# Kernel tuning notes

Hardware: AMD Instinct MI355X
Metric: run time of the kernel (lower is better)

## Reference

```python
import jax, jax.numpy as jnp
import numpy as np
import math

N_HEADS = 16


def setup_inputs() -> dict:
    key = jax.random.key(0)
    ks = jax.random.split(key, 8)
    B, N, H = 4, 1024, 1024
    hidden_states = jax.random.normal(ks[0], (B, N, H), dtype=jnp.float32)
    # per-sample valid length in [N//2, N]; padding_vector is nonzero on valid
    # positions, zero afterwards (first zero index defines the pad boundary)
    lengths = jax.random.randint(ks[1], (B,), N // 2, N + 1)
    padding_vector = (jnp.arange(N)[None, :] < lengths[:, None]).astype(jnp.int32)
    s = 0.02
    Wq = jax.random.normal(ks[2], (H, H), dtype=jnp.float32) * s
    Wk = jax.random.normal(ks[3], (H, H), dtype=jnp.float32) * s
    Wv = jax.random.normal(ks[4], (H, H), dtype=jnp.float32) * s
    bq = jnp.zeros((H,), dtype=jnp.float32)
    bk = jnp.zeros((H,), dtype=jnp.float32)
    bv = jnp.zeros((H,), dtype=jnp.float32)
    return dict(hidden_states=hidden_states, padding_vector=padding_vector,
                Wq=Wq, bq=bq, Wk=Wk, bk=bk, Wv=Wv, bv=bv, max_n_codes=N)


def _heads(x, n_heads):
    B, N, H = x.shape
    return x.reshape(B, N, n_heads, H // n_heads).transpose(0, 2, 1, 3)  # (B,h,N,d)


def reference(hidden_states, padding_vector, Wq, bq, Wk, bk, Wv, bv, max_n_codes):
    B, N, H = hidden_states.shape
    d = H // N_HEADS
    q = _heads(hidden_states @ Wq.T + bq, N_HEADS)  # (B,h,N,d)
    k = _heads(hidden_states @ Wk.T + bk, N_HEADS)
    v = _heads(hidden_states @ Wv.T + bv, N_HEADS)
    scores = jnp.einsum('bhnd,bhmd->bhnm', q, k) / math.sqrt(d)
    # padd = index of first zero in padding_vector, or N if no zero
    is_zero = padding_vector == 0
    padd = jnp.where(is_zero.any(axis=1), jnp.argmax(is_zero, axis=1), N)  # (B,)
    idx = jnp.arange(N)
    valid = idx[None, :] < padd[:, None]                      # (B,N)
    keep = valid[:, None, :, None] & valid[:, None, None, :]  # (B,1,N,N)
    # masked positions get -inf pre-softmax, then are zeroed post-softmax.
    # finfo.min instead of -inf keeps fully-masked rows NaN-free; they are
    # zeroed by the post-softmax mask exactly as in the torch version.
    neg = jnp.finfo(scores.dtype).min
    probs = jax.nn.softmax(jnp.where(keep, scores, neg), axis=-1)
    probs = jnp.where(keep, probs, 0.0)
    attention_values = probs.sum(axis=-2)                     # (B,h,N)
    context = jnp.einsum('bhnm,bhmd->bhnd', probs, v)
    return (attention_values, k, q, context, scores)
```

## Files before the change

kernel.cpp:

```cpp
#include <hip/hip_runtime.h>
#include <math.h>

#define B_ 4
#define N_ 1024
#define H_ 1024
#define NH_ 16
#define D_ 64

#define SZ_ATTN (B_*NH_*N_)
#define SZ_HEADS (B_*NH_*N_*D_)

#define XT_CHUNKS (32*16*1024)
#define WT_CHUNKS (8*16*1024)

typedef __attribute__((ext_vector_type(8))) short short8v;
typedef __attribute__((ext_vector_type(4))) short short4v;
typedef __attribute__((ext_vector_type(4))) float floatx4;

typedef __attribute__((address_space(1))) const unsigned int gau32;
typedef __attribute__((address_space(3))) unsigned int lau32;

__device__ inline void gl16(const unsigned short* g, unsigned short* l) {
    __builtin_amdgcn_global_load_lds((gau32*)g, (lau32*)l, 16, 0, 0);
}

__device__ inline unsigned short f2bf(float x) {
    union { float f; unsigned int u; } v; v.f = x;
    unsigned int r = v.u + 0x7FFFu + ((v.u >> 16) & 1u);
    return (unsigned short)(r >> 16);
}
__device__ inline float bf2f(unsigned short u) {
    union { unsigned int i; float f; } v; v.i = ((unsigned int)u) << 16;
    return v.f;
}

__global__ void padd_kernel(const int* __restrict__ pv, int* __restrict__ padd) {
    __shared__ int mn;
    const int b = blockIdx.x;
    if (threadIdx.x == 0) mn = N_;
    __syncthreads();
    for (int m = threadIdx.x; m < N_; m += blockDim.x)
        if (pv[b*N_ + m] == 0) atomicMin(&mn, m);
    __syncthreads();
    if (threadIdx.x == 0) padd[b] = mn;
}

__global__ __launch_bounds__(256)
void convert_kernel(const float* __restrict__ X,  const float* __restrict__ Wq,
                    const float* __restrict__ Wk, const float* __restrict__ Wv,
                    unsigned short* __restrict__ scratch)
{
    const int g = blockIdx.x*256 + threadIdx.x;
    const float* src;
    if (g < XT_CHUNKS) {
        const int c = g & 1023, t = g >> 10;
        const int it = t >> 4, kt = t & 15;
        const int row = c >> 3, kcs = c & 7, kc = kcs ^ (row & 7);
        src = X + (size_t)(it*128 + row)*H_ + kt*64 + kc*8;
    } else {
        const int gw = g - XT_CHUNKS;
        const int which = gw >> 17;
        const int rem = gw & (WT_CHUNKS-1);
        const int c = rem & 1023, t = rem >> 10;
        const int jt = t >> 4, kt = t & 15;
        const int row = c >> 3, kcs = c & 7, kc = kcs ^ (row & 7);
        const float* W = (which == 0) ? Wq : (which == 1) ? Wk : Wv;
        src = W + (size_t)(jt*128 + row)*H_ + kt*64 + kc*8;
    }
    const float4 a = *(const float4*)src;
    const float4 b = *(const float4*)(src + 4);
    short8v pk;
    pk[0] = (short)f2bf(a.x); pk[1] = (short)f2bf(a.y);
    pk[2] = (short)f2bf(a.z); pk[3] = (short)f2bf(a.w);
    pk[4] = (short)f2bf(b.x); pk[5] = (short)f2bf(b.y);
    pk[6] = (short)f2bf(b.z); pk[7] = (short)f2bf(b.w);
    *(short8v*)(scratch + (size_t)g*8) = pk;
}

__global__ __launch_bounds__(256)
void proj3_mfma_kernel(const unsigned short* __restrict__ Xt,
                       const unsigned short* __restrict__ Wt_all,
                       const float* __restrict__ bq_, const float* __restrict__ bk_,
                       const float* __restrict__ bv_,
                       float* __restrict__ Oq, float* __restrict__ Ok,
                       float* __restrict__ Ov)
{
    const int which = blockIdx.z;
    const unsigned short* __restrict__ Wt = Wt_all + (size_t)which*WT_CHUNKS*8;
    const float* __restrict__ bias = (which == 0) ? bq_ : (which == 1) ? bk_ : bv_;
    float* __restrict__ outH       = (which == 0) ? Oq  : (which == 1) ? Ok  : Ov;

    __shared__ __align__(16) unsigned short Abf[128*64];
    __shared__ __align__(16) unsigned short Bbf[128*64];

    const int tid  = threadIdx.x;
    const int lane = tid & 63;
    const int w    = tid >> 6;
    const int wr   = w >> 1, wc = w & 1;
    const int fr   = lane & 15, hi = lane >> 4;
    const int i0 = blockIdx.y * 128;
    const int j0 = blockIdx.x * 128;

    floatx4 acc[4][4];
    #pragma unroll
    for (int mi = 0; mi < 4; ++mi)
        #pragma unroll
        for (int ni = 0; ni < 4; ++ni)
            acc[mi][ni] = (floatx4){0.f, 0.f, 0.f, 0.f};

    for (int ktile = 0; ktile < 16; ++ktile) {
        __syncthreads();
        const unsigned short* xsrc = Xt + (size_t)(blockIdx.y*16 + ktile)*8192;
        const unsigned short* wsrc = Wt + (size_t)(blockIdx.x*16 + ktile)*8192;
        #pragma unroll
        for (int l = 0; l < 4; ++l) {
            const int ch = l*256 + tid;
            gl16(xsrc + (size_t)ch*8, Abf + (size_t)ch*8);
            gl16(wsrc + (size_t)ch*8, Bbf + (size_t)ch*8);
        }
        __syncthreads();

        #pragma unroll
        for (int ks = 0; ks < 2; ++ks) {
            short8v a[4], b[4];
            #pragma unroll
            for (int mi = 0; mi < 4; ++mi) {
                const int row = wr*64 + mi*16 + fr;
                a[mi] = *(const short8v*)&Abf[row*64 + (((ks*4 + hi) ^ (fr & 7)) << 3)];
            }
            #pragma unroll
            for (int ni = 0; ni < 4; ++ni) {
                const int row = wc*64 + ni*16 + fr;
                b[ni] = *(const short8v*)&Bbf[row*64 + (((ks*4 + hi) ^ (fr & 7)) << 3)];
            }
            #pragma unroll
            for (int mi = 0; mi < 4; ++mi)
                #pragma unroll
                for (int ni = 0; ni < 4; ++ni)
                    acc[mi][ni] = __builtin_amdgcn_mfma_f32_16x16x32_bf16(
                        a[mi], b[ni], acc[mi][ni], 0, 0, 0);
        }
    }

    #pragma unroll
    for (int ni = 0; ni < 4; ++ni) {
        const int j = j0 + wc*64 + ni*16 + fr;
        const int head = j >> 6, d = j & 63;
        const float bvj = bias[j];
        #pragma unroll
        for (int mi = 0; mi < 4; ++mi) {
            #pragma unroll
            for (int reg = 0; reg < 4; ++reg) {
                const int i = i0 + wr*64 + mi*16 + hi*4 + reg;
                const int bb = i >> 10, n = i & 1023;
                outH[((size_t)(bb*NH_ + head)*N_ + n)*D_ + d] = acc[mi][ni][reg] + bvj;
            }
        }
    }
}

__global__ __launch_bounds__(256)
void fused_attn_mfma(const float* __restrict__ Q, const float* __restrict__ K,
                     const float* __restrict__ Vh, const int* __restrict__ padd,
                     float* __restrict__ S, float* __restrict__ ctx,
                     float* __restrict__ attn)
{
    __shared__ __align__(16) unsigned short Abf[128*64];
    __shared__ __align__(16) unsigned short Bbf[64*64];
    __shared__ float smx[128], sinv[128];
    __shared__ float cred[256];

    const int tid  = threadIdx.x;
    const int lane = tid & 63;
    const int w    = tid >> 6;
    const int fr   = lane & 15, hi = lane >> 4;
    const int bh = blockIdx.y;
    const int n0 = blockIdx.x * 128;
    const int b  = bh >> 4;
    const int pd = padd[b];
    const float* Qb = Q  + (size_t)bh*N_*D_;
    const float* Kb = K  + (size_t)bh*N_*D_;
    const float* Vb = Vh + (size_t)bh*N_*D_;
    float* Sb = S + (size_t)bh*N_*N_;

    #pragma unroll
    for (int l = 0; l < 4; ++l) {
        const int e = tid + 256*l;
        const int row = e >> 3, kc = e & 7;
        const float* src = Qb + (size_t)(n0+row)*D_ + kc*8;
        const float4 xa = *(const float4*)(src);
        const float4 xb = *(const float4*)(src + 4);
        short8v pk;
        pk[0] = (short)f2bf(xa.x); pk[1] = (short)f2bf(xa.y);
        pk[2] = (short)f2bf(xa.z); pk[3] = (short)f2bf(xa.w);
        pk[4] = (short)f2bf(xb.x); pk[5] = (short)f2bf(xb.y);
        pk[6] = (short)f2bf(xb.z); pk[7] = (short)f2bf(xb.w);
        *(short8v*)&Abf[row*64 + ((kc ^ (row & 7)) << 3)] = pk;
    }
    __syncthreads();

    short8v qa[2][2];
    #pragma unroll
    for (int mi = 0; mi < 2; ++mi)
        #pragma unroll
        for (int ks = 0; ks < 2; ++ks) {
            const int arow = w*32 + mi*16 + fr;
            qa[mi][ks] = *(const short8v*)&Abf[arow*64 + (((ks*4 + hi) ^ (fr & 7)) << 3)];
        }

    float run_mx[2][4], run_sm[2][4];
    #pragma unroll
    for (int mi = 0; mi < 2; ++mi)
        #pragma unroll
        for (int reg = 0; reg < 4; ++reg) { run_mx[mi][reg] = -INFINITY; run_sm[mi][reg] = 0.f; }

    for (int m0 = 0; m0 < N_; m0 += 64) {
        #pragma unroll
        for (int l = 0; l < 2; ++l) {
            const int e = tid + 256*l;
            const int row = e >> 3, kc = e & 7;
            const float* src = Kb + (size_t)(m0+row)*D_ + kc*8;
            const float4 xa = *(const float4*)(src);
            const float4 xb = *(const float4*)(src + 4);
            short8v pk;
            pk[0] = (short)f2bf(xa.x); pk[1] = (short)f2bf(xa.y);
            pk[2] = (short)f2bf(xa.z); pk[3] = (short)f2bf(xa.w);
            pk[4] = (short)f2bf(xb.x); pk[5] = (short)f2bf(xb.y);
            pk[6] = (short)f2bf(xb.z); pk[7] = (short)f2bf(xb.w);
            *(short8v*)&Bbf[row*64 + ((kc ^ (row & 7)) << 3)] = pk;
        }
        __syncthreads();

        floatx4 sacc[2][4];
        #pragma unroll
        for (int mi = 0; mi < 2; ++mi)
            #pragma unroll
            for (int ni = 0; ni < 4; ++ni)
                sacc[mi][ni] = (floatx4){0.f, 0.f, 0.f, 0.f};

        #pragma unroll
        for (int ks = 0; ks < 2; ++ks) {
            short8v kb[4];
            #pragma unroll
            for (int ni = 0; ni < 4; ++ni) {
                const int brow = ni*16 + fr;
                kb[ni] = *(const short8v*)&Bbf[brow*64 + (((ks*4 + hi) ^ (fr & 7)) << 3)];
            }
            #pragma unroll
            for (int mi = 0; mi < 2; ++mi)
                #pragma unroll
                for (int ni = 0; ni < 4; ++ni)
                    sacc[mi][ni] = __builtin_amdgcn_mfma_f32_16x16x32_bf16(
                        qa[mi][ks], kb[ni], sacc[mi][ni], 0, 0, 0);
        }

        #pragma unroll
        for (int mi = 0; mi < 2; ++mi)
            #pragma unroll
            for (int ni = 0; ni < 4; ++ni) {
                sacc[mi][ni] *= 0.125f;
                const int m = m0 + ni*16 + fr;
                #pragma unroll
                for (int reg = 0; reg < 4; ++reg) {
                    const int n = n0 + w*32 + mi*16 + hi*4 + reg;
                    Sb[(size_t)n*N_ + m] = sacc[mi][ni][reg];
                }
            }

        if (m0 < pd) {
            #pragma unroll
            for (int mi = 0; mi < 2; ++mi)
                #pragma unroll
                for (int reg = 0; reg < 4; ++reg) {
                    float tm = -INFINITY;
                    #pragma unroll
                    for (int ni = 0; ni < 4; ++ni)
                        if (m0 + ni*16 + fr < pd) tm = fmaxf(tm, sacc[mi][ni][reg]);
                    tm = fmaxf(tm, __shfl_xor(tm, 1, 64));
                    tm = fmaxf(tm, __shfl_xor(tm, 2, 64));
                    tm = fmaxf(tm, __shfl_xor(tm, 4, 64));
                    tm = fmaxf(tm, __shfl_xor(tm, 8, 64));
                    const float nm = fmaxf(run_mx[mi][reg], tm);
                    float s = 0.f;
                    #pragma unroll
                    for (int ni = 0; ni < 4; ++ni)
                        if (m0 + ni*16 + fr < pd) s += __expf(sacc[mi][ni][reg] - nm);
                    s += __shfl_xor(s, 1, 64);
                    s += __shfl_xor(s, 2, 64);
                    s += __shfl_xor(s, 4, 64);
                    s += __shfl_xor(s, 8, 64);
                    run_sm[mi][reg] = run_sm[mi][reg]*__expf(run_mx[mi][reg] - nm) + s;
                    run_mx[mi][reg] = nm;
                }
        }
        __syncthreads();
    }

    if (n0 >= pd) {
        #pragma unroll
        for (int l = 0; l < 8; ++l) {
            const int e = tid + 256*l;
            const int row = e >> 4, c4 = e & 15;
            float4 z; z.x = z.y = z.z = z.w = 0.f;
            *(float4*)(ctx + ((size_t)bh*N_ + n0 + row)*D_ + c4*4) = z;
        }
        return;
    }

    if (fr == 0) {
        #pragma unroll
        for (int mi = 0; mi < 2; ++mi)
            #pragma unroll
            for (int reg = 0; reg < 4; ++reg) {
                const int row = w*32 + mi*16 + hi*4 + reg;
                const bool v = (n0 + row) < pd;
                smx[row]  = v ? run_mx[mi][reg] : 0.f;
                sinv[row] = v ? 1.f/run_sm[mi][reg] : 0.f;
            }
    }
    __syncthreads();

    floatx4 acc2[2][4];
    #pragma unroll
    for (int mi = 0; mi < 2; ++mi)
        #pragma unroll
        for (int ni = 0; ni < 4; ++ni)
            acc2[mi][ni] = (floatx4){0.f, 0.f, 0.f, 0.f};

    for (int m0 = 0; m0 < pd; m0 += 64) {
        #pragma unroll
        for (int l = 0; l < 8; ++l) {
            const int e = tid + 256*l;
            const int row = e >> 4, c4 = e & 15;
            const int n = n0 + row;
            const int m = m0 + c4*4;
            const float4 s4 = *(const float4*)(Sb + (size_t)n*N_ + m);
            const bool rv = n < pd;
            const float fmx = smx[row], fiv = sinv[row];
            short4v pk;
            pk[0] = (short)f2bf((rv && m+0 < pd) ? __expf(s4.x - fmx)*fiv : 0.f);
            pk[1] = (short)f2bf((rv && m+1 < pd) ? __expf(s4.y - fmx)*fiv : 0.f);
            pk[2] = (short)f2bf((rv && m+2 < pd) ? __expf(s4.z - fmx)*fiv : 0.f);
            pk[3] = (short)f2bf((rv && m+3 < pd) ? __expf(s4.w - fmx)*fiv : 0.f);
            const int elem = row*64 + (((c4 >> 1) ^ (row & 7)) << 3) + (c4 & 1)*4;
            *(short4v*)&Abf[elem] = pk;
        }
        {
            const int d = tid & 63, mg = tid >> 6;
            #pragma unroll
            for (int jj = 0; jj < 2; ++jj) {
                short8v pk;
                #pragma unroll
                for (int j = 0; j < 8; ++j)
                    pk[j] = (short)f2bf(Vb[(size_t)(m0 + mg*16 + jj*8 + j)*D_ + d]);
                const int chunk = mg*2 + jj;
                *(short8v*)&Bbf[d*64 + ((chunk ^ (d & 7)) << 3)] = pk;
            }
        }
        __syncthreads();

        {
            const int ml = tid & 63, q = tid >> 6;
            float cs = 0.f;
            #pragma unroll
            for (int i = 0; i < 32; ++i) {
                const int row = q*32 + i;
                cs += bf2f(Abf[row*64 + (((ml >> 3) ^ (row & 7)) << 3) + (ml & 7)]);
            }
            cred[tid] = cs;
        }
        __syncthreads();
        if (tid < 64) {
            const float vtot = cred[tid] + cred[tid+64] + cred[tid+128] + cred[tid+192];
            atomicAdd(&attn[(size_t)bh*N_ + m0 + tid], vtot);
        }

        #pragma unroll
        for (int ks = 0; ks < 2; ++ks) {
            short8v a[2], vfr[4];
            #pragma unroll
            for (int mi = 0; mi < 2; ++mi) {
                const int arow = w*32 + mi*16 + fr;
                a[mi] = *(const short8v*)&Abf[arow*64 + (((ks*4 + hi) ^ (fr & 7)) << 3)];
            }
            #pragma unroll
            for (int ni = 0; ni < 4; ++ni) {
                const int bd = ni*16 + fr;
                vfr[ni] = *(const short8v*)&Bbf[bd*64 + (((ks*4 + hi) ^ (fr & 7)) << 3)];
            }
            #pragma unroll
            for (int mi = 0; mi < 2; ++mi)
                #pragma unroll
                for (int ni = 0; ni < 4; ++ni)
                    acc2[mi][ni] = __builtin_amdgcn_mfma_f32_16x16x32_bf16(
                        a[mi], vfr[ni], acc2[mi][ni], 0, 0, 0);
        }
        __syncthreads();
    }

    #pragma unroll
    for (int mi = 0; mi < 2; ++mi)
        #pragma unroll
        for (int ni = 0; ni < 4; ++ni) {
            const int d = ni*16 + fr;
            #pragma unroll
            for (int reg = 0; reg < 4; ++reg) {
                const int n = n0 + w*32 + mi*16 + hi*4 + reg;
                ctx[((size_t)bh*N_ + n)*D_ + d] = acc2[mi][ni][reg];
            }
        }
}

extern "C" void kernel_launch(void* const* d_in, const int* in_sizes, int n_in,
                              void* d_out, int out_size, void* d_ws, size_t ws_size,
                              hipStream_t stream)
{
    const float* hs = (const float*)d_in[0];
    const int*   pv = (const int*)d_in[1];
    const float* Wq = (const float*)d_in[2];
    const float* bq = (const float*)d_in[3];
    const float* Wk = (const float*)d_in[4];
    const float* bk = (const float*)d_in[5];
    const float* Wv = (const float*)d_in[6];
    const float* bv = (const float*)d_in[7];
    float* out = (float*)d_out;

    float* out_attn = out;
    float* out_k    = out_attn + SZ_ATTN;
    float* out_q    = out_k + SZ_HEADS;
    float* out_ctx  = out_q + SZ_HEADS;
    float* out_sc   = out_ctx + SZ_HEADS;

    int*   padd = (int*)d_ws;
    float* v_ws = (float*)((char*)d_ws + 256);

    unsigned short* scratch = (unsigned short*)out_sc;
    const unsigned short* Xt = scratch;
    const unsigned short* Wt = scratch + (size_t)XT_CHUNKS*8;

    hipMemsetAsync(out_attn, 0, SZ_ATTN*sizeof(float), stream);
    padd_kernel<<<B_, 256, 0, stream>>>(pv, padd);

    convert_kernel<<<(XT_CHUNKS + 3*WT_CHUNKS)/256, 256, 0, stream>>>(
        hs, Wq, Wk, Wv, scratch);

    dim3 pg(H_/128, (B_*N_)/128, 3);
    proj3_mfma_kernel<<<pg, 256, 0, stream>>>(Xt, Wt, bq, bk, bv,
                                              out_q, out_k, v_ws);

    dim3 fg(N_/128, B_*NH_);
    fused_attn_mfma<<<fg, 256, 0, stream>>>(out_q, out_k, v_ws, padd,
                                            out_sc, out_ctx, out_attn);
}
```

Baseline: 492.4 us.

## Recompute QK^T in the PV pass and stage score stores through LDS

The second pass no longer reads the materialized score matrix back from global memory. It reloads K tiles, recomputes the scores with MFMA, and applies exp and normalisation in registers before the PV product. In the first pass, score tiles are staged in a padded LDS buffer so the global writes of S become coalesced float4 row stores. This trades a large global re-read of S for extra MFMA work and about 67KB of LDS per block, which may lower occupancy. Row masking for rows past the pad boundary now relies on the stored row max and inverse-sum values.

New measurement: 470.7 us. -4.4%, faster.

```diff
diff --git a/kernel.cpp b/kernel.cpp
--- a/kernel.cpp
+++ b/kernel.cpp
@@ -14,7 +14,6 @@
 #define WT_CHUNKS (8*16*1024)
 
 typedef __attribute__((ext_vector_type(8))) short short8v;
-typedef __attribute__((ext_vector_type(4))) short short4v;
 typedef __attribute__((ext_vector_type(4))) float floatx4;
 
 typedef __attribute__((address_space(1))) const unsigned int gau32;
@@ -165,8 +164,10 @@
                      float* __restrict__ S, float* __restrict__ ctx,
                      float* __restrict__ attn)
 {
-    __shared__ __align__(16) unsigned short Abf[128*64];
-    __shared__ __align__(16) unsigned short Bbf[64*64];
+    __shared__ __align__(16) unsigned short Qbf[128*64];
+    __shared__ __align__(16) unsigned short Kbf[64*64];
+    __shared__ __align__(16) unsigned short Vbf[64*64];
+    __shared__ float Sst[128*68];
     __shared__ float smx[128], sinv[128];
     __shared__ float cred[256];
 
@@ -195,7 +196,7 @@
         pk[2] = (short)f2bf(xa.z); pk[3] = (short)f2bf(xa.w);
         pk[4] = (short)f2bf(xb.x); pk[5] = (short)f2bf(xb.y);
         pk[6] = (short)f2bf(xb.z); pk[7] = (short)f2bf(xb.w);
-        *(short8v*)&Abf[row*64 + ((kc ^ (row & 7)) << 3)] = pk;
+        *(short8v*)&Qbf[row*64 + ((kc ^ (row & 7)) << 3)] = pk;
     }
     __syncthreads();
 
@@ -205,8 +206,9 @@
         #pragma unroll
         for (int ks = 0; ks < 2; ++ks) {
             const int arow = w*32 + mi*16 + fr;
-            qa[mi][ks] = *(const short8v*)&Abf[arow*64 + (((ks*4 + hi) ^ (fr & 7)) << 3)];
-        }
+            qa[mi][ks] = *(const short8v*)&Qbf[arow*64 + (((ks*4 + hi) ^ (fr & 7)) << 3)];
+        }
+    __syncthreads();
 
     float run_mx[2][4], run_sm[2][4];
     #pragma unroll
@@ -227,7 +229,7 @@
             pk[2] = (short)f2bf(xa.z); pk[3] = (short)f2bf(xa.w);
             pk[4] = (short)f2bf(xb.x); pk[5] = (short)f2bf(xb.y);
             pk[6] = (short)f2bf(xb.z); pk[7] = (short)f2bf(xb.w);
-            *(short8v*)&Bbf[row*64 + ((kc ^ (row & 7)) << 3)] = pk;
+            *(short8v*)&Kbf[row*64 + ((kc ^ (row & 7)) << 3)] = pk;
         }
         __syncthreads();
 
@@ -244,7 +246,7 @@
             #pragma unroll
             for (int ni = 0; ni < 4; ++ni) {
                 const int brow = ni*16 + fr;
-                kb[ni] = *(const short8v*)&Bbf[brow*64 + (((ks*4 + hi) ^ (fr & 7)) << 3)];
+                kb[ni] = *(const short8v*)&Kbf[brow*64 + (((ks*4 + hi) ^ (fr & 7)) << 3)];
             }
             #pragma unroll
             for (int mi = 0; mi < 2; ++mi)
@@ -259,11 +261,11 @@
             #pragma unroll
             for (int ni = 0; ni < 4; ++ni) {
                 sacc[mi][ni] *= 0.125f;
-                const int m = m0 + ni*16 + fr;
+                const int m = ni*16 + fr;
                 #pragma unroll
                 for (int reg = 0; reg < 4; ++reg) {
-                    const int n = n0 + w*32 + mi*16 + hi*4 + reg;
-                    Sb[(size_t)n*N_ + m] = sacc[mi][ni][reg];
+                    const int row = w*32 + mi*16 + hi*4 + reg;
+                    Sst[row*68 + m] = sacc[mi][ni][reg];
                 }
             }
 
@@ -294,6 +296,14 @@
                 }
         }
         __syncthreads();
+
+        #pragma unroll
+        for (int l = 0; l < 8; ++l) {
+            const int e = tid + 256*l;
+            const int row = e >> 4, c4 = e & 15;
+            const float4 v = *(const float4*)&Sst[row*68 + c4*4];
+            *(float4*)(Sb + (size_t)(n0+row)*N_ + m0 + c4*4) = v;
+        }
     }
 
     if (n0 >= pd) {
@@ -320,6 +330,16 @@
     }
     __syncthreads();
 
+    float mxr[2][4], ivr[2][4];
+    #pragma unroll
+    for (int mi = 0; mi < 2; ++mi)
+        #pragma unroll
+        for (int reg = 0; reg < 4; ++reg) {
+            const int row = w*32 + mi*16 + hi*4 + reg;
+            mxr[mi][reg] = smx[row];
+            ivr[mi][reg] = sinv[row];
+        }
+
     floatx4 acc2[2][4];
     #pragma unroll
     for (int mi = 0; mi < 2; ++mi)
@@ -329,21 +349,18 @@
 
     for (int m0 = 0; m0 < pd; m0 += 64) {
         #pragma unroll
-        for (int l = 0; l < 8; ++l) {
+        for (int l = 0; l < 2; ++l) {
             const int e = tid + 256*l;
-            const int row = e >> 4, c4 = e & 15;
-            const int n = n0 + row;
-            const int m = m0 + c4*4;
-            const float4 s4 = *(const float4*)(Sb + (size_t)n*N_ + m);
-            const bool rv = n < pd;
-            const float fmx = smx[row], fiv = sinv[row];
-            short4v pk;
-            pk[0] = (short)f2bf((rv && m+0 < pd) ? __expf(s4.x - fmx)*fiv : 0.f);
-            pk[1] = (short)f2bf((rv && m+1 < pd) ? __expf(s4.y - fmx)*fiv : 0.f);
-            pk[2] = (short)f2bf((rv && m+2 < pd) ? __expf(s4.z - fmx)*fiv : 0.f);
-            pk[3] = (short)f2bf((rv && m+3 < pd) ? __expf(s4.w - fmx)*fiv : 0.f);
-            const int elem = row*64 + (((c4 >> 1) ^ (row & 7)) << 3) + (c4 & 1)*4;
-            *(short4v*)&Abf[elem] = pk;
+            const int row = e >> 3, kc = e & 7;
+            const float* src = Kb + (size_t)(m0+row)*D_ + kc*8;
+            const float4 xa = *(const float4*)(src);
+            const float4 xb = *(const float4*)(src + 4);
+            short8v pk;
+            pk[0] = (short)f2bf(xa.x); pk[1] = (short)f2bf(xa.y);
+            pk[2] = (short)f2bf(xa.z); pk[3] = (short)f2bf(xa.w);
+            pk[4] = (short)f2bf(xb.x); pk[5] = (short)f2bf(xb.y);
+            pk[6] = (short)f2bf(xb.z); pk[7] = (short)f2bf(xb.w);
+            *(short8v*)&Kbf[row*64 + ((kc ^ (row & 7)) << 3)] = pk;
         }
         {
             const int d = tid & 63, mg = tid >> 6;
@@ -354,10 +371,70 @@
                 for (int j = 0; j < 8; ++j)
                     pk[j] = (short)f2bf(Vb[(size_t)(m0 + mg*16 + jj*8 + j)*D_ + d]);
                 const int chunk = mg*2 + jj;
-                *(short8v*)&Bbf[d*64 + ((chunk ^ (d & 7)) << 3)] = pk;
-            }
-        }
-        __syncthreads();
+                *(short8v*)&Vbf[d*64 + ((chunk ^ (d & 7)) << 3)] = pk;
+            }
+        }
+        __syncthreads();
+
+        floatx4 sacc[2][4];
+        #pragma unroll
+        for (int mi = 0; mi < 2; ++mi)
+            #pragma unroll
+            for (int ni = 0; ni < 4; ++ni)
+                sacc[mi][ni] = (floatx4){0.f, 0.f, 0.f, 0.f};
+
+        #pragma unroll
+        for (int ks = 0; ks < 2; ++ks) {
+            short8v kb[4];
+            #pragma unroll
+            for (int ni = 0; ni < 4; ++ni) {
+                const int brow = ni*16 + fr;
+                kb[ni] = *(const short8v*)&Kbf[brow*64 + (((ks*4 + hi) ^ (fr & 7)) << 3)];
+            }
+            #pragma unroll
+            for (int mi = 0; mi < 2; ++mi)
+                #pragma unroll
+                for (int ni = 0; ni < 4; ++ni)
+                    sacc[mi][ni] = __builtin_amdgcn_mfma_f32_16x16x32_bf16(
+                        qa[mi][ks], kb[ni], sacc[mi][ni], 0, 0, 0);
+        }
+
+        #pragma unroll
+        for (int mi = 0; mi < 2; ++mi)
+            #pragma unroll
+            for (int ni = 0; ni < 4; ++ni) {
+                const int mloc = ni*16 + fr;
+                const bool mok = (m0 + mloc) < pd;
+                #pragma unroll
+                for (int reg = 0; reg < 4; ++reg) {
+                    const int row = w*32 + mi*16 + hi*4 + reg;
+                    float p = __expf(sacc[mi][ni][reg]*0.125f - mxr[mi][reg]) * ivr[mi][reg];
+                    if (!mok) p = 0.f;
+                    Qbf[row*64 + (((mloc >> 3) ^ (row & 7)) << 3) + (mloc & 7)] = f2bf(p);
+                }
+            }
+        __syncthreads();
+
+        #pragma unroll
+        for (int ks = 0; ks < 2; ++ks) {
+            short8v a[2], vfr[4];
+            #pragma unroll
+            for (int mi = 0; mi < 2; ++mi) {
+                const int arow = w*32 + mi*16 + fr;
+                a[mi] = *(const short8v*)&Qbf[arow*64 + (((ks*4 + hi) ^ (fr & 7)) << 3)];
+            }
+            #pragma unroll
+            for (int ni = 0; ni < 4; ++ni) {
+                const int bd = ni*16 + fr;
+                vfr[ni] = *(const short8v*)&Vbf[bd*64 + (((ks*4 + hi) ^ (fr & 7)) << 3)];
+            }
+            #pragma unroll
+            for (int mi = 0; mi < 2; ++mi)
+                #pragma unroll
+                for (int ni = 0; ni < 4; ++ni)
+                    acc2[mi][ni] = __builtin_amdgcn_mfma_f32_16x16x32_bf16(
+                        a[mi], vfr[ni], acc2[mi][ni], 0, 0, 0);
+        }
 
         {
             const int ml = tid & 63, q = tid >> 6;
@@ -365,7 +442,7 @@
             #pragma unroll
             for (int i = 0; i < 32; ++i) {
                 const int row = q*32 + i;
-                cs += bf2f(Abf[row*64 + (((ml >> 3) ^ (row & 7)) << 3) + (ml & 7)]);
+                cs += bf2f(Qbf[row*64 + (((ml >> 3) ^ (row & 7)) << 3) + (ml & 7)]);
             }
             cred[tid] = cs;
         }
@@ -374,28 +451,6 @@
             const float vtot = cred[tid] + cred[tid+64] + cred[tid+128] + cred[tid+192];
             atomicAdd(&attn[(size_t)bh*N_ + m0 + tid], vtot);
         }
-
-        #pragma unroll
-        for (int ks = 0; ks < 2; ++ks) {
-            short8v a[2], vfr[4];
-            #pragma unroll
-            for (int mi = 0; mi < 2; ++mi) {
-                const int arow = w*32 + mi*16 + fr;
-                a[mi] = *(const short8v*)&Abf[arow*64 + (((ks*4 + hi) ^ (fr & 7)) << 3)];
-            }
-            #pragma unroll
-            for (int ni = 0; ni < 4; ++ni) {
-                const int bd = ni*16 + fr;
-                vfr[ni] = *(const short8v*)&Bbf[bd*64 + (((ks*4 + hi) ^ (fr & 7)) << 3)];
-            }
-            #pragma unroll
-            for (int mi = 0; mi < 2; ++mi)
-                #pragma unroll
-                for (int ni = 0; ni < 4; ++ni)
-                    acc2[mi][ni] = __builtin_amdgcn_mfma_f32_16x16x32_bf16(
-                        a[mi], vfr[ni], acc2[mi][ni], 0, 0, 0);
-        }
-        __syncthreads();
     }
 
     #pragma unroll
```
